# Kernel optimization log

Hardware: AMD Instinct MI355X
Metric: run time of the kernel (lower is better)

Reference implementation:

```python
import jax, jax.numpy as jnp
import numpy as np

TEMP = 0.07      # InfoNCE temperature
NB = 15          # neighborhood side length
HALF = NB // 2
NUM_SAMPLES = 256
EPS = 1e-8       # F.cosine_similarity eps


def setup_inputs() -> dict:
    key = jax.random.key(0)
    k1, k2, k3, k4 = jax.random.split(key, 4)
    B, D, H, W = 8, 128, 256, 256
    features = jax.random.normal(k1, (B, D, H, W), jnp.float32)
    targets = jax.random.randint(k2, (B, H, W), 0, 4, jnp.int32)
    # anchors restricted to the valid interior [HALF, H-HALF)
    anchor_h = jax.random.randint(k3, (B, NUM_SAMPLES), HALF, H - HALF, jnp.int32)
    anchor_w = jax.random.randint(k4, (B, NUM_SAMPLES), HALF, W - HALF, jnp.int32)
    return {"features": features, "targets": targets,
            "anchor_h": anchor_h, "anchor_w": anchor_w}


def _local_contrastive_loss(features, targets, anchor_h, anchor_w):
    offs = jnp.arange(-HALF, HALF + 1)  # (NB,)

    def per_image(feat, lab, ah, aw):
        # feat: (D,H,W), lab: (H,W), ah/aw: (N,)
        N = ah.shape[0]
        wh = jnp.broadcast_to(ah[:, None, None] + offs[None, :, None], (N, NB, NB))
        ww = jnp.broadcast_to(aw[:, None, None] + offs[None, None, :], (N, NB, NB))
        patch = feat[:, wh, ww]          # (D, N, NB, NB) gathered local windows
        plab = lab[wh, ww]               # (N, NB, NB)
        af = feat[:, ah, aw]             # (D, N) anchor features
        alab = lab[ah, aw]               # (N,)
        # cosine similarity (with eps clamp like F.cosine_similarity), / temperature
        an = jnp.maximum(jnp.sqrt(jnp.sum(af * af, axis=0)), EPS)          # (N,)
        pn = jnp.maximum(jnp.sqrt(jnp.sum(patch * patch, axis=0)), EPS)    # (N,NB,NB)
        sim = jnp.einsum('dn,dnkl->nkl', af, patch) / (an[:, None, None] * pn) / TEMP
        # positive mask: same label, centre pixel excluded
        pos = plab == alab[:, None, None]
        pos = pos.at[:, HALF, HALF].set(False)
        sim_flat = sim.reshape(N, -1)                 # (N, NB*NB)
        pos_flat = pos.reshape(N, -1)
        pos_cnt = pos_flat.sum(-1)                    # (N,)
        lse = jax.nn.logsumexp(sim_flat, axis=-1)     # (N,)
        pos_mean = jnp.where(pos_flat, sim_flat, 0.0).sum(-1) / jnp.maximum(pos_cnt, 1)
        valid = pos_cnt > 0
        loss_i = -(pos_mean - lse)
        return jnp.where(valid, loss_i, 0.0).sum(), valid.sum()

    losses, counts = jax.vmap(per_image)(features, targets, anchor_h, anchor_w)
    total = losses.sum()
    cnt = counts.sum()
    return jnp.where(cnt > 0,
                     total / jnp.maximum(cnt, 1).astype(total.dtype),
                     jnp.zeros((), total.dtype))


def reference(features, targets, anchor_h, anchor_w):
    return _local_contrastive_loss(features, targets, anchor_h, anchor_w)
```

## Files before the change

kernel.cpp:

```cpp
#include <hip/hip_runtime.h>
#include <math.h>

#define TEMPC   0.07f
#define NBK     15
#define HALFK   7
#define NPOS    225
#define DD      128
#define HHH     256
#define WWW     256
#define PLANE   (HHH * WWW)
#define EPSC    1e-8f

__global__ __launch_bounds__(256) void lcl_main(
    const float* __restrict__ feat,
    const int*   __restrict__ targ,
    const int*   __restrict__ anch_h,
    const int*   __restrict__ anch_w,
    float*       __restrict__ loss_part,
    float*       __restrict__ cnt_part)
{
    const int bn   = blockIdx.x;
    const int b    = bn >> 8;
    const int tid  = threadIdx.x;
    const int lane = tid & 63;
    const int wave = tid >> 6;

    __shared__ float af[DD];
    __shared__ float red[4], red2[4], red3[4];
    __shared__ float s_an;
    __shared__ float s_max;

    const int ah = anch_h[bn];
    const int aw = anch_w[bn];
    const int* lab = targ + b * PLANE;
    const int alab = lab[ah * WWW + aw];
    const float* fb = feat + (size_t)b * DD * PLANE;

    float sqa = 0.f;
    if (tid < DD) {
        float v = fb[(size_t)tid * PLANE + ah * WWW + aw];
        af[tid] = v;
        sqa = v * v;
    }
    #pragma unroll
    for (int off = 32; off; off >>= 1) sqa += __shfl_down(sqa, off, 64);
    if (lane == 0) red[wave] = sqa;
    __syncthreads();
    if (tid == 0) s_an = fmaxf(sqrtf(red[0] + red[1] + red[2] + red[3]), EPSC);
    __syncthreads();
    const float an = s_an;

    const bool active = tid < NPOS;
    float dot = 0.f, sq = 0.f;
    int hh = 0, ww = 0;
    if (active) {
        const int k = tid / NBK;
        const int l = tid - k * NBK;
        hh = ah - HALFK + k;
        ww = aw - HALFK + l;
        const float* p = fb + hh * WWW + ww;
        #pragma unroll 16
        for (int d = 0; d < DD; ++d) {
            float v = p[d * PLANE];
            dot = fmaf(af[d], v, dot);
            sq  = fmaf(v,     v, sq);
        }
    }

    float sim = -INFINITY;
    bool  pos = false;
    if (active) {
        float pn = fmaxf(sqrtf(sq), EPSC);
        sim = dot / (an * pn * TEMPC);
        pos = (lab[hh * WWW + ww] == alab) && (tid != (HALFK * NBK + HALFK));
    }

    float m = sim;
    #pragma unroll
    for (int off = 32; off; off >>= 1) m = fmaxf(m, __shfl_down(m, off, 64));
    if (lane == 0) red[wave] = m;
    __syncthreads();
    if (tid == 0) s_max = fmaxf(fmaxf(red[0], red[1]), fmaxf(red[2], red[3]));
    __syncthreads();
    m = s_max;

    float e  = active ? expf(sim - m) : 0.f;
    float ps = pos ? sim : 0.f;
    float pc = pos ? 1.f : 0.f;
    #pragma unroll
    for (int off = 32; off; off >>= 1) {
        e  += __shfl_down(e,  off, 64);
        ps += __shfl_down(ps, off, 64);
        pc += __shfl_down(pc, off, 64);
    }
    if (lane == 0) { red[wave] = e; red2[wave] = ps; red3[wave] = pc; }
    __syncthreads();
    if (tid == 0) {
        float E  = red[0]  + red[1]  + red[2]  + red[3];
        float PS = red2[0] + red2[1] + red2[2] + red2[3];
        float PC = red3[0] + red3[1] + red3[2] + red3[3];
        float lse = m + logf(E);
        bool valid = PC > 0.5f;
        loss_part[bn] = valid ? (lse - PS / PC) : 0.f;
        cnt_part[bn]  = valid ? 1.f : 0.f;
    }
}

__global__ __launch_bounds__(256) void lcl_finalize(
    const float* __restrict__ loss_part,
    const float* __restrict__ cnt_part,
    float*       __restrict__ out,
    int n)
{
    const int tid  = threadIdx.x;
    const int lane = tid & 63;
    const int wave = tid >> 6;
    __shared__ float rs[4], rc[4];

    float s = 0.f, c = 0.f;
    for (int i = tid; i < n; i += 256) {
        s += loss_part[i];
        c += cnt_part[i];
    }
    #pragma unroll
    for (int off = 32; off; off >>= 1) {
        s += __shfl_down(s, off, 64);
        c += __shfl_down(c, off, 64);
    }
    if (lane == 0) { rs[wave] = s; rc[wave] = c; }
    __syncthreads();
    if (tid == 0) {
        float S = rs[0] + rs[1] + rs[2] + rs[3];
        float C = rc[0] + rc[1] + rc[2] + rc[3];
        out[0] = (C > 0.5f) ? (S / C) : 0.f;
    }
}

extern "C" void kernel_launch(void* const* d_in, const int* in_sizes, int n_in,
                              void* d_out, int out_size, void* d_ws, size_t ws_size,
                              hipStream_t stream) {
    const float* feat  = (const float*)d_in[0];
    const int*   targ  = (const int*)d_in[1];
    const int*   anchh = (const int*)d_in[2];
    const int*   anchw = (const int*)d_in[3];
    float* out = (float*)d_out;

    const int n_anchors = in_sizes[2];

    float* loss_part = (float*)d_ws;
    float* cnt_part  = loss_part + n_anchors;

    lcl_main<<<n_anchors, 256, 0, stream>>>(feat, targ, anchh, anchw,
                                            loss_part, cnt_part);
    lcl_finalize<<<1, 256, 0, stream>>>(loss_part, cnt_part, out, n_anchors);
}
```

Measured before the change: 377.4 us.

## Split patch dot products into float4 column groups and channel chunks

Each thread now loads four adjacent columns as an unaligned float4 over a 32-channel chunk. The four channel chunks are spread across 240 threads, and partial dot and squared-norm sums go to shared memory, where they are combined per position. The 15-wide row is covered by four overlapping quads, with the duplicated column masked out. This aims to give more independent loads in flight per thread, wider memory transactions and shorter serial loops. The cost is extra shared-memory traffic and one more barrier, and the float4 loads may be misaligned.

```diff
diff --git a/kernel.cpp b/kernel.cpp
--- a/kernel.cpp
+++ b/kernel.cpp
@@ -4,12 +4,19 @@
 #define TEMPC   0.07f
 #define NBK     15
 #define HALFK   7
-#define NPOS    225
 #define DD      128
 #define HHH     256
 #define WWW     256
 #define PLANE   (HHH * WWW)
 #define EPSC    1e-8f
+
+#define NQ      60
+#define NCHUNK  4
+#define DCH     32
+#define NP2     (NQ * NCHUNK)
+#define NPP     240
+
+typedef float f4 __attribute__((ext_vector_type(4), aligned(4)));
 
 __global__ __launch_bounds__(256) void lcl_main(
     const float* __restrict__ feat,
@@ -26,6 +33,8 @@
     const int wave = tid >> 6;
 
     __shared__ float af[DD];
+    __shared__ float pd[NCHUNK * NPP];
+    __shared__ float pq[NCHUNK * NPP];
     __shared__ float red[4], red2[4], red3[4];
     __shared__ float s_an;
     __shared__ float s_max;
@@ -48,31 +57,51 @@
     __syncthreads();
     if (tid == 0) s_an = fmaxf(sqrtf(red[0] + red[1] + red[2] + red[3]), EPSC);
     __syncthreads();
+
+    if (tid < NP2) {
+        const int c  = tid / NQ;
+        const int q  = tid - c * NQ;
+        const int k  = q >> 2;
+        const int ql = q & 3;
+        const int colb = (ql < 3) ? (ql << 2) : 11;
+        const int hh = ah - HALFK + k;
+        const int ww = aw - HALFK + colb;
+        const float* p = fb + (size_t)(c * DCH) * PLANE + (hh * WWW + ww);
+        const float* a = &af[c * DCH];
+        float d0 = 0.f, d1 = 0.f, d2 = 0.f, d3 = 0.f;
+        float s0 = 0.f, s1 = 0.f, s2 = 0.f, s3 = 0.f;
+        #pragma unroll 8
+        for (int i = 0; i < DCH; ++i) {
+            f4 v = *reinterpret_cast<const f4*>(p + i * PLANE);
+            float av = a[i];
+            d0 = fmaf(av, v[0], d0);  s0 = fmaf(v[0], v[0], s0);
+            d1 = fmaf(av, v[1], d1);  s1 = fmaf(v[1], v[1], s1);
+            d2 = fmaf(av, v[2], d2);  s2 = fmaf(v[2], v[2], s2);
+            d3 = fmaf(av, v[3], d3);  s3 = fmaf(v[3], v[3], s3);
+        }
+        const int base = c * NPP + (q << 2);
+        pd[base + 0] = d0; pd[base + 1] = d1; pd[base + 2] = d2; pd[base + 3] = d3;
+        pq[base + 0] = s0; pq[base + 1] = s1; pq[base + 2] = s2; pq[base + 3] = s3;
+    }
+    __syncthreads();
+
     const float an = s_an;
-
-    const bool active = tid < NPOS;
-    float dot = 0.f, sq = 0.f;
-    int hh = 0, ww = 0;
-    if (active) {
-        const int k = tid / NBK;
-        const int l = tid - k * NBK;
-        hh = ah - HALFK + k;
-        ww = aw - HALFK + l;
-        const float* p = fb + hh * WWW + ww;
-        #pragma unroll 16
-        for (int d = 0; d < DD; ++d) {
-            float v = p[d * PLANE];
-            dot = fmaf(af[d], v, dot);
-            sq  = fmaf(v,     v, sq);
-        }
-    }
-
     float sim = -INFINITY;
     bool  pos = false;
-    if (active) {
-        float pn = fmaxf(sqrtf(sq), EPSC);
-        sim = dot / (an * pn * TEMPC);
-        pos = (lab[hh * WWW + ww] == alab) && (tid != (HALFK * NBK + HALFK));
+    if (tid < NPP) {
+        const int ql = (tid >> 2) & 3;
+        const int j  = tid & 3;
+        if (!(ql == 3 && j == 0)) {
+            const int k   = tid >> 4;
+            const int col = ((ql < 3) ? (ql << 2) : 11) + j;
+            float dot = pd[tid] + pd[NPP + tid] + pd[2 * NPP + tid] + pd[3 * NPP + tid];
+            float sq  = pq[tid] + pq[NPP + tid] + pq[2 * NPP + tid] + pq[3 * NPP + tid];
+            float pn = fmaxf(sqrtf(sq), EPSC);
+            sim = dot / (an * pn * TEMPC);
+            const int hh = ah - HALFK + k;
+            const int wp = aw - HALFK + col;
+            pos = (lab[hh * WWW + wp] == alab) && !(k == HALFK && col == HALFK);
+        }
     }
 
     float m = sim;
@@ -84,7 +113,7 @@
     __syncthreads();
     m = s_max;
 
-    float e  = active ? expf(sim - m) : 0.f;
+    float e  = expf(sim - m);
     float ps = pos ? sim : 0.f;
     float pc = pos ? 1.f : 0.f;
     #pragma unroll
```

New measurement: 379.1 us. About the same (+0.5%).
